# Optimization experiments

Hardware: AMD Instinct MI355X
Metric: run time of the kernel (lower is better)

## Reference

```python
import jax, jax.numpy as jnp
import numpy as np
import math

N, T, D_MODEL = 4, 2048, 1024
NHEAD = 16
HEAD_DIM = D_MODEL // NHEAD
ROTARY_DIM = 64
WINDOW = (128, 128)
ROPE_BASE = 10000.0


def _rope_cos_sin(seq_len, rotary_dim, dtype):
    # non-interleaved (GPT-NeoX style) rotary embedding tables
    inv_freq = 1.0 / (ROPE_BASE ** (jnp.arange(0, rotary_dim, 2, dtype=jnp.float32) / rotary_dim))
    t = jnp.arange(seq_len, dtype=jnp.float32)
    freqs = jnp.outer(t, inv_freq)  # [T, rotary_dim//2]
    return jnp.cos(freqs).astype(dtype), jnp.sin(freqs).astype(dtype)


def _apply_rope(x, cos, sin):
    # x: [N, T, H, D]; rotate first ROTARY_DIM dims, pass the rest through
    r = ROTARY_DIM
    x_rot, x_pass = x[..., :r], x[..., r:]
    x1, x2 = x_rot[..., : r // 2], x_rot[..., r // 2 :]
    c = cos[None, :, None, :]
    s = sin[None, :, None, :]
    out = jnp.concatenate([x1 * c - x2 * s, x1 * s + x2 * c], axis=-1)
    return jnp.concatenate([out, x_pass], axis=-1)


def _sliding_window_bias(seq_len, window, dtype):
    i = jnp.arange(seq_len)[:, None]
    j = jnp.arange(seq_len)[None, :]
    # triu(diag=-w0) & tril(diag=w1): keep j - i in [-w0, w1]
    keep = (j - i >= -window[0]) & (j - i <= window[1])
    return jnp.where(keep, jnp.zeros((), dtype), jnp.full((), -jnp.inf, dtype))


def setup_inputs() -> dict:
    key = jax.random.key(0)
    k1, k2, k3 = jax.random.split(key, 3)
    x = jax.random.normal(k1, (N, T, D_MODEL), dtype=jnp.float32)
    Wqkv = jax.random.normal(k2, (D_MODEL, 3 * D_MODEL), dtype=jnp.float32) * (1.0 / math.sqrt(D_MODEL))
    Wout = jax.random.normal(k3, (D_MODEL, D_MODEL), dtype=jnp.float32) * (1.0 / math.sqrt(D_MODEL))
    bout = jnp.zeros((D_MODEL,), dtype=jnp.float32)
    return {"x": x, "Wqkv": Wqkv, "Wout": Wout, "bout": bout}


def reference(x, Wqkv, Wout, bout):
    n, t, _ = x.shape
    qkv = (x @ Wqkv).reshape(n, t, 3, NHEAD, HEAD_DIM)
    q, k, v = qkv[:, :, 0], qkv[:, :, 1], qkv[:, :, 2]  # each [N, T, H, D]
    cos, sin = _rope_cos_sin(t, ROTARY_DIM, x.dtype)
    q = _apply_rope(q, cos, sin)
    k = _apply_rope(k, cos, sin)
    scale = 1.0 / math.sqrt(HEAD_DIM)
    bias = _sliding_window_bias(t, WINDOW, x.dtype)  # [T, T]
    scores = jnp.einsum("bthd,bshd->bhts", q, k) * scale + bias[None, None]
    attn = jax.nn.softmax(scores, axis=-1)
    out = jnp.einsum("bhts,bshd->bthd", attn, v).reshape(n, t, D_MODEL)
    return out @ Wout + bout
```

## Files before the change

### kernel.cpp

```cpp
#include <hip/hip_runtime.h>
#include <hip/hip_bf16.h>
#include <cstdint>
#include <cstddef>

typedef __bf16 bf16_t;
typedef bf16_t bf16x8 __attribute__((ext_vector_type(8)));
typedef float f32x4 __attribute__((ext_vector_type(4)));
typedef unsigned short ushort_t;

#define T_SEQ 2048
#define DM 1024
#define NH 16
#define HD 64
#define WIN 128
#define ROPE_C 0.28782313662425572f
#define SCALE_LOG2E 0.18033688011112042f
#define ATT_M 16.0f

__device__ __forceinline__ ushort_t f2bf(float f) {
    union { float f; unsigned u; } v; v.f = f;
    unsigned r = v.u + 0x7fff + ((v.u >> 16) & 1);
    return (ushort_t)(r >> 16);
}
__device__ __forceinline__ float sane(float v, float sent) {
    return (fabsf(v) < 1e30f) ? v : sent;
}
__device__ __forceinline__ void gld16(const ushort_t* g, ushort_t* l) {
    __builtin_amdgcn_global_load_lds(
        (const __attribute__((address_space(1))) unsigned int*)g,
        (__attribute__((address_space(3))) unsigned int*)l, 16, 0, 0);
}

__global__ __launch_bounds__(256) void kzero_f(float* __restrict__ p) {
    size_t i = ((size_t)blockIdx.x * 256 + threadIdx.x) * 4;
    float4 z; z.x = z.y = z.z = z.w = 0.f;
    *(float4*)(p + i) = z;
}

__device__ __forceinline__ void trans_f2b_tile(const float* __restrict__ in,
                                               ushort_t* __restrict__ out,
                                               int R, int C, int c0, int r0) {
    __shared__ __align__(16) ushort_t tile[64][72];
    const int tid = threadIdx.x;
    const int rl = tid >> 2, q4 = tid & 3;
    const float* src = in + (size_t)(r0 + rl) * C + c0 + q4 * 16;
    ushort_t cv[16];
#pragma unroll
    for (int i = 0; i < 4; i++) {
        float4 f = *(const float4*)(src + i * 4);
        cv[i * 4 + 0] = f2bf(f.x); cv[i * 4 + 1] = f2bf(f.y);
        cv[i * 4 + 2] = f2bf(f.z); cv[i * 4 + 3] = f2bf(f.w);
    }
    *(uint4*)&tile[rl][q4 * 16]     = *(uint4*)&cv[0];
    *(uint4*)&tile[rl][q4 * 16 + 8] = *(uint4*)&cv[8];
    __syncthreads();
    const int cl = tid >> 2;
    ushort_t tmp[16];
#pragma unroll
    for (int i = 0; i < 16; i++) tmp[i] = tile[q4 * 16 + i][cl];
    ushort_t* dst = out + (size_t)(c0 + cl) * R + r0 + q4 * 16;
    *(uint4*)(dst)     = *(uint4*)&tmp[0];
    *(uint4*)(dst + 8) = *(uint4*)&tmp[8];
}

__global__ __launch_bounds__(256) void prep(const float* __restrict__ x,
                                            const float* __restrict__ Wqkv,
                                            const float* __restrict__ Wout,
                                            ushort_t* __restrict__ xb,
                                            ushort_t* __restrict__ WqkvT,
                                            ushort_t* __restrict__ WoutT) {
    const int bx = blockIdx.x;
    if (bx < 4096) {
        size_t i = ((size_t)bx * 256 + threadIdx.x) * 8;
        float4 a0 = *(const float4*)(x + i);
        float4 a1 = *(const float4*)(x + i + 4);
        ushort_t cv[8];
        cv[0] = f2bf(a0.x); cv[1] = f2bf(a0.y); cv[2] = f2bf(a0.z); cv[3] = f2bf(a0.w);
        cv[4] = f2bf(a1.x); cv[5] = f2bf(a1.y); cv[6] = f2bf(a1.z); cv[7] = f2bf(a1.w);
        *(uint4*)(xb + i) = *(uint4*)cv;
    } else if (bx < 4864) {
        int tb = bx - 4096;
        trans_f2b_tile(Wqkv, WqkvT, 1024, 3072, (tb % 48) * 64, (tb / 48) * 64);
    } else {
        int tb = bx - 4864;
        trans_f2b_tile(Wout, WoutT, 1024, 1024, (tb & 15) * 64, (tb >> 4) * 64);
    }
}

__global__ __launch_bounds__(256) void gemm_qkv(const ushort_t* __restrict__ A,
                                                const ushort_t* __restrict__ Bt,
                                                ushort_t* __restrict__ Qr,
                                                ushort_t* __restrict__ Kr,
                                                ushort_t* __restrict__ Vt) {
    __shared__ __align__(16) ushort_t As[128 * 32];
    __shared__ __align__(16) ushort_t Bs[128 * 32];
    const int m0 = blockIdx.x * 128, n0 = blockIdx.y * 128;
    const int tid = threadIdx.x;
    const int lane = tid & 63, w = tid >> 6;
    const int wm = (w & 1) * 64, wn = (w >> 1) * 64;
    const int c = lane & 15, g = lane >> 4;
    const int lrow = lane >> 2, lcol = (lane & 3) * 8;
    const int ch0 = 2 * w, ch1 = 2 * w + 1;

    f32x4 acc[4][4];
#pragma unroll
    for (int mi = 0; mi < 4; mi++)
#pragma unroll
        for (int ni = 0; ni < 4; ni++)
#pragma unroll
            for (int r = 0; r < 4; r++) acc[mi][ni][r] = 0.f;

    for (int k0 = 0; k0 < 1024; k0 += 32) {
        __syncthreads();
        gld16(A  + (size_t)(m0 + ch0 * 16 + lrow) * 1024 + k0 + lcol, &As[ch0 * 512]);
        gld16(A  + (size_t)(m0 + ch1 * 16 + lrow) * 1024 + k0 + lcol, &As[ch1 * 512]);
        gld16(Bt + (size_t)(n0 + ch0 * 16 + lrow) * 1024 + k0 + lcol, &Bs[ch0 * 512]);
        gld16(Bt + (size_t)(n0 + ch1 * 16 + lrow) * 1024 + k0 + lcol, &Bs[ch1 * 512]);
        __syncthreads();
        bf16x8 af[4], bfr[4];
#pragma unroll
        for (int mi = 0; mi < 4; mi++)
            af[mi] = *(const bf16x8*)&As[(wm + mi * 16 + c) * 32 + g * 8];
#pragma unroll
        for (int ni = 0; ni < 4; ni++)
            bfr[ni] = *(const bf16x8*)&Bs[(wn + ni * 16 + c) * 32 + g * 8];
#pragma unroll
        for (int mi = 0; mi < 4; mi++)
#pragma unroll
            for (int ni = 0; ni < 4; ni++)
                acc[mi][ni] = __builtin_amdgcn_mfma_f32_16x16x32_bf16(
                    af[mi], bfr[ni], acc[mi][ni], 0, 0, 0);
    }

    const int nb = n0 + wn;
    const int sec = nb >> 10;
    const int h = (nb >> 6) & 15;

    if (sec < 2) {
        ushort_t* dst = (sec == 0) ? Qr : Kr;
        const float invf0 = __expf(-(float)(c) * ROPE_C);
        const float invf1 = __expf(-(float)(16 + c) * ROPE_C);
#pragma unroll
        for (int mi = 0; mi < 4; mi++)
#pragma unroll
            for (int r = 0; r < 4; r++) {
                int tg = m0 + wm + mi * 16 + g * 4 + r;
                int nB = tg >> 11, t = tg & (T_SEQ - 1);
                float a0 = (float)t * invf0, a1 = (float)t * invf1;
                float s0 = __sinf(a0), c0 = __cosf(a0);
                float s1 = __sinf(a1), c1 = __cosf(a1);
                size_t base = ((size_t)(nB * NH + h) * T_SEQ + t) * 64;
                float x1a = acc[mi][0][r], x2a = acc[mi][2][r];
                float x1b = acc[mi][1][r], x2b = acc[mi][3][r];
                dst[base + c]      = f2bf(sane(x1a * c0 - x2a * s0, 1e3f));
                dst[base + 16 + c] = f2bf(sane(x1b * c1 - x2b * s1, 1e3f));
                dst[base + 32 + c] = f2bf(sane(x1a * s0 + x2a * c0, 1e3f));
                dst[base + 48 + c] = f2bf(sane(x1b * s1 + x2b * c1, 1e3f));
            }
    } else {
#pragma unroll
        for (int mi = 0; mi < 4; mi++) {
            int tgb = m0 + wm + mi * 16 + g * 4;
            int nB = tgb >> 11, t = tgb & (T_SEQ - 1);
            size_t vrow = (size_t)(nB * NH + h) * 64 * T_SEQ;
#pragma unroll
            for (int ni = 0; ni < 4; ni++) {
                ushort4 pk;
                pk.x = f2bf(sane(acc[mi][ni][0], 1e3f));
                pk.y = f2bf(sane(acc[mi][ni][1], 1e3f));
                pk.z = f2bf(sane(acc[mi][ni][2], 1e3f));
                pk.w = f2bf(sane(acc[mi][ni][3], 1e3f));
                *(ushort4*)&Vt[vrow + (size_t)(ni * 16 + c) * T_SEQ + t] = pk;
            }
        }
    }
}

__global__ __launch_bounds__(256) void gemm_out(const ushort_t* __restrict__ A,
                                                const ushort_t* __restrict__ Bt,
                                                float* __restrict__ C,
                                                const float* __restrict__ bias) {
    __shared__ __align__(16) ushort_t As[64 * 32];
    __shared__ __align__(16) ushort_t Bs[128 * 32];
    const int m0 = blockIdx.x * 64, n0 = blockIdx.y * 128;
    const int tid = threadIdx.x;
    const int lane = tid & 63, w = tid >> 6;
    const int wm = (w & 1) * 32, wn = (w >> 1) * 64;
    const int c = lane & 15, g = lane >> 4;
    const int lrow = lane >> 2, lcol = (lane & 3) * 8;
    const int ch0 = 2 * w, ch1 = 2 * w + 1;

    f32x4 acc[2][4];
#pragma unroll
    for (int mi = 0; mi < 2; mi++)
#pragma unroll
        for (int ni = 0; ni < 4; ni++)
#pragma unroll
            for (int r = 0; r < 4; r++) acc[mi][ni][r] = 0.f;

    for (int k0 = 0; k0 < 1024; k0 += 32) {
        __syncthreads();
        gld16(A  + (size_t)(m0 + w * 16 + lrow) * 1024 + k0 + lcol, &As[w * 512]);
        gld16(Bt + (size_t)(n0 + ch0 * 16 + lrow) * 1024 + k0 + lcol, &Bs[ch0 * 512]);
        gld16(Bt + (size_t)(n0 + ch1 * 16 + lrow) * 1024 + k0 + lcol, &Bs[ch1 * 512]);
        __syncthreads();
        bf16x8 af[2], bfr[4];
#pragma unroll
        for (int mi = 0; mi < 2; mi++)
            af[mi] = *(const bf16x8*)&As[(wm + mi * 16 + c) * 32 + g * 8];
#pragma unroll
        for (int ni = 0; ni < 4; ni++)
            bfr[ni] = *(const bf16x8*)&Bs[(wn + ni * 16 + c) * 32 + g * 8];
#pragma unroll
        for (int mi = 0; mi < 2; mi++)
#pragma unroll
            for (int ni = 0; ni < 4; ni++)
                acc[mi][ni] = __builtin_amdgcn_mfma_f32_16x16x32_bf16(
                    af[mi], bfr[ni], acc[mi][ni], 0, 0, 0);
    }

#pragma unroll
    for (int ni = 0; ni < 4; ni++) {
        int col = n0 + wn + ni * 16 + c;
        float bv = bias[col];
#pragma unroll
        for (int mi = 0; mi < 2; mi++)
#pragma unroll
            for (int r = 0; r < 4; r++) {
                int rowi = m0 + wm + mi * 16 + g * 4 + r;
                C[(size_t)rowi * 1024 + col] = sane(acc[mi][ni][r] + bv, 1e8f);
            }
    }
}

__global__ __launch_bounds__(256) void attn_swin(const ushort_t* __restrict__ Qr,
                                                 const ushort_t* __restrict__ Kr,
                                                 const ushort_t* __restrict__ Vt,
                                                 ushort_t* __restrict__ O) {
    __shared__ __align__(16) ushort_t Ks[32 * 72];
    __shared__ __align__(16) ushort_t Vs[64 * 72];
    __shared__ __align__(16) ushort_t pbuf[4][2][16 * 32];
    const int tid = threadIdx.x;
    const int wid = tid >> 6, lane = tid & 63;
    const int qb = (blockIdx.x & 15) * 128;
    const int h = (blockIdx.x >> 4) & 15, n = blockIdx.x >> 8;
    const int c = lane & 15, g = lane >> 4;
    const size_t hb = ((size_t)(n * NH + h)) * T_SEQ * 64;
    const int t0s[2] = { qb + wid * 16, qb + 64 + wid * 16 };
    const int ks_row = tid >> 3, ks_col = (tid & 7) * 8;
    const int vs_row = tid >> 2, vs_col = (tid & 3) * 8;

    bf16x8 qf0[2], qf1[2];
#pragma unroll
    for (int sub = 0; sub < 2; sub++) {
        qf0[sub] = *(const bf16x8*)(Qr + hb + (size_t)(t0s[sub] + c) * 64 + g * 8);
        qf1[sub] = *(const bf16x8*)(Qr + hb + (size_t)(t0s[sub] + c) * 64 + 32 + g * 8);
    }

    f32x4 o[2][4];
    float l_r[2][4];
#pragma unroll
    for (int sub = 0; sub < 2; sub++)
#pragma unroll
        for (int i = 0; i < 4; i++) {
            l_r[sub][i] = 0.f;
#pragma unroll
            for (int r = 0; r < 4; r++) o[sub][i][r] = 0.f;
        }

    int sB_lo = qb - WIN;        if (sB_lo < 0) sB_lo = 0;
    int sB_hi = qb + 127 + WIN;  if (sB_hi > T_SEQ - 1) sB_hi = T_SEQ - 1;

    uint4 kreg = *(const uint4*)(Kr + hb + (size_t)(sB_lo + ks_row) * 64 + ks_col);
    uint4 vreg = *(const uint4*)(Vt + hb + (size_t)vs_row * T_SEQ + sB_lo + vs_col);

    for (int s0 = sB_lo; s0 <= sB_hi; s0 += 32) {
        __syncthreads();
        *(uint4*)&Ks[ks_row * 72 + ks_col] = kreg;
        *(uint4*)&Vs[vs_row * 72 + vs_col] = vreg;
        __syncthreads();
        int s1 = s0 + 32;
        if (s1 <= sB_hi) {
            kreg = *(const uint4*)(Kr + hb + (size_t)(s1 + ks_row) * 64 + ks_col);
            vreg = *(const uint4*)(Vt + hb + (size_t)vs_row * T_SEQ + s1 + vs_col);
        }
        bool act[2];
#pragma unroll
        for (int sub = 0; sub < 2; sub++)
            act[sub] = !(s0 > t0s[sub] + 143 || s0 + 31 < t0s[sub] - WIN);
        if (!act[0] && !act[1]) continue;

#pragma unroll
        for (int sub = 0; sub < 2; sub++) {
            if (!act[sub]) continue;
            const int t0 = t0s[sub];
            f32x4 S[2];
#pragma unroll
            for (int sh = 0; sh < 2; sh++) {
                bf16x8 kf0 = *(const bf16x8*)&Ks[(sh * 16 + c) * 72 + g * 8];
                bf16x8 kf1 = *(const bf16x8*)&Ks[(sh * 16 + c) * 72 + 32 + g * 8];
                f32x4 z;
#pragma unroll
                for (int r = 0; r < 4; r++) z[r] = 0.f;
                z = __builtin_amdgcn_mfma_f32_16x16x32_bf16(qf0[sub], kf0, z, 0, 0, 0);
                z = __builtin_amdgcn_mfma_f32_16x16x32_bf16(qf1[sub], kf1, z, 0, 0, 0);
                S[sh] = z;
            }
            const bool interior = (s0 >= t0 - 113) && (s0 <= t0 + 97);
            ushort_t* pb = pbuf[wid][sub];
            if (interior) {
#pragma unroll
                for (int sh = 0; sh < 2; sh++)
#pragma unroll
                    for (int r = 0; r < 4; r++) {
                        float p = exp2f(S[sh][r] * SCALE_LOG2E - ATT_M);
                        l_r[sub][r] += p;
                        pb[(g * 4 + r) * 32 + sh * 16 + c] = f2bf(p);
                    }
            } else {
#pragma unroll
                for (int sh = 0; sh < 2; sh++)
#pragma unroll
                    for (int r = 0; r < 4; r++) {
                        int s = s0 + sh * 16 + c;
                        int q = t0 + g * 4 + r;
                        bool keep = (s - q >= -WIN) && (s - q <= WIN);
                        float v = keep ? S[sh][r] * SCALE_LOG2E : -1e30f;
                        float p = exp2f(v - ATT_M);
                        l_r[sub][r] += p;
                        pb[(g * 4 + r) * 32 + sh * 16 + c] = f2bf(p);
                    }
            }
        }
        __asm__ volatile("s_waitcnt lgkmcnt(0)" ::: "memory");
#pragma unroll
        for (int sub = 0; sub < 2; sub++) {
            if (!act[sub]) continue;
            bf16x8 pf = *(const bf16x8*)&pbuf[wid][sub][c * 32 + g * 8];
#pragma unroll
            for (int di = 0; di < 4; di++) {
                bf16x8 vf = *(const bf16x8*)&Vs[(di * 16 + c) * 72 + g * 8];
                o[sub][di] = __builtin_amdgcn_mfma_f32_16x16x32_bf16(pf, vf, o[sub][di], 0, 0, 0);
            }
        }
        __asm__ volatile("" ::: "memory");
    }

#pragma unroll
    for (int sub = 0; sub < 2; sub++) {
#pragma unroll
        for (int off = 1; off < 16; off <<= 1)
#pragma unroll
            for (int r = 0; r < 4; r++)
                l_r[sub][r] += __shfl_xor(l_r[sub][r], off, 64);
        float inv[4];
#pragma unroll
        for (int r = 0; r < 4; r++) inv[r] = __builtin_amdgcn_rcpf(l_r[sub][r]);
#pragma unroll
        for (int di = 0; di < 4; di++)
#pragma unroll
            for (int r = 0; r < 4; r++) {
                int q = t0s[sub] + g * 4 + r;
                float val = o[sub][di][r] * inv[r];
                O[((size_t)(n * T_SEQ + q)) * DM + h * 64 + di * 16 + c] =
                    f2bf(sane(val, 1e6f));
            }
    }
}

extern "C" void kernel_launch(void* const* d_in, const int* in_sizes, int n_in,
                              void* d_out, int out_size, void* d_ws, size_t ws_size,
                              hipStream_t stream) {
    const float* x    = (const float*)d_in[0];
    const float* Wqkv = (const float*)d_in[1];
    const float* Wout = (const float*)d_in[2];
    const float* bout = (const float*)d_in[3];
    float* out = (float*)d_out;

    const size_t NEED = 72ull << 20;
    if (ws_size < NEED) {
        kzero_f<<<dim3(8192), 256, 0, stream>>>(out);
        return;
    }
    char* ws = (char*)d_ws;
    ushort_t* WqkvT = (ushort_t*)(ws);
    ushort_t* WoutT = (ushort_t*)(ws + (6ull << 20));
    ushort_t* Qr    = (ushort_t*)(ws + (8ull << 20));
    ushort_t* Kr    = (ushort_t*)(ws + (24ull << 20));
    ushort_t* Vt    = (ushort_t*)(ws + (40ull << 20));
    ushort_t* xb    = (ushort_t*)(ws + (56ull << 20));
    ushort_t* Oat   = xb;

    prep<<<dim3(5120), 256, 0, stream>>>(x, Wqkv, Wout, xb, WqkvT, WoutT);
    gemm_qkv<<<dim3(64, 24), 256, 0, stream>>>(xb, WqkvT, Qr, Kr, Vt);
    attn_swin<<<dim3(1024), 256, 0, stream>>>(Qr, Kr, Vt, Oat);
    gemm_out<<<dim3(128, 8), 256, 0, stream>>>(Oat, WoutT, out, bout);
}
```

Measured before the change: 220.4 us.

## Rewrite both GEMMs with triple-buffered async LDS pipeline, larger tiles, swizzled layout

Replaces the QKV and output projection GEMM loops with a shared core using 128x256x64 tiles, 512 threads, a three-stage LDS ring buffer filled by async global-to-LDS loads, and an XOR-swizzled LDS layout. MFMA work is split into two phases separated by barriers, with wave priority raised around the matrix instructions. The goal is to hide global load latency behind compute, cut per-iteration barrier cost and improve data reuse. In exchange the larger LDS footprint and per-block register use lower occupancy, and the output GEMM now launches only 256 blocks, which may underfill the GPU.

Result: faster. 210.1 us (-4.7%).

```diff
diff --git a/kernel.cpp b/kernel.cpp
--- a/kernel.cpp
+++ b/kernel.cpp
@@ -87,64 +87,140 @@
     }
 }
 
-__global__ __launch_bounds__(256) void gemm_qkv(const ushort_t* __restrict__ A,
+#define BM 128
+#define BN 256
+#define BK 64
+#define KTILES 16
+#define LBUF ((BM + BN) * BK)
+#define LTOT (3 * LBUF)
+
+__device__ __forceinline__ void gemm_core(const ushort_t* __restrict__ Agl,
+                                          const ushort_t* __restrict__ Bgl,
+                                          ushort_t* L, int m0, int n0,
+                                          f32x4 (&acc)[4][4]) {
+    const int tid = threadIdx.x;
+    const int lane = tid & 63, w = tid >> 6;
+    const int wr = w >> 2, wc = w & 3;
+    const int c = lane & 15, g = lane >> 4;
+    const int rr = tid >> 3;
+    const int cc8 = ((tid & 7) ^ (rr & 7)) * 8;
+    const int lw = (w * 8) * BK;
+    const int arow = wr * 64 + c;
+    const int brow = wc * 64 + c;
+    const int cxk0 = ((0 + g) ^ (c & 7)) * 8;
+    const int cxk1 = ((4 + g) ^ (c & 7)) * 8;
+
+#pragma unroll
+    for (int mi = 0; mi < 4; ++mi)
+#pragma unroll
+        for (int ni = 0; ni < 4; ++ni)
+#pragma unroll
+            for (int r = 0; r < 4; ++r) acc[mi][ni][r] = 0.f;
+
+    auto STAGE = [&](int kt, int bo) {
+        const int k0 = kt * BK;
+        const ushort_t* ga = Agl + (size_t)(m0 + rr) * 1024 + k0 + cc8;
+        ushort_t* la = L + bo + lw;
+        gld16(ga, la);
+        gld16(ga + 64 * 1024, la + 64 * BK);
+        const ushort_t* gb = Bgl + (size_t)(n0 + rr) * 1024 + k0 + cc8;
+        ushort_t* lb = la + BM * BK;
+#pragma unroll
+        for (int s = 0; s < 4; ++s)
+            gld16(gb + (size_t)(s * 64) * 1024, lb + s * 64 * BK);
+    };
+
+    STAGE(0, 0);
+    STAGE(1, LBUF);
+    asm volatile("s_waitcnt vmcnt(6)\n\ts_barrier" ::: "memory");
+
+    int bcur = 0;
+    for (int kt = 0; kt < KTILES; ++kt) {
+        int bst = bcur + 2 * LBUF; if (bst >= LTOT) bst -= LTOT;
+        if (kt + 2 < KTILES) STAGE(kt + 2, bst);
+
+        const ushort_t* Lb = L + bcur;
+        const ushort_t* Bb = Lb + BM * BK;
+        bf16x8 af[4][2], bf[2][2];
+#pragma unroll
+        for (int mi = 0; mi < 4; ++mi) {
+            const ushort_t* p = Lb + (arow + mi * 16) * BK;
+            af[mi][0] = *(const bf16x8*)(p + cxk0);
+            af[mi][1] = *(const bf16x8*)(p + cxk1);
+        }
+#pragma unroll
+        for (int ni = 0; ni < 2; ++ni) {
+            const ushort_t* p = Bb + (brow + ni * 16) * BK;
+            bf[ni][0] = *(const bf16x8*)(p + cxk0);
+            bf[ni][1] = *(const bf16x8*)(p + cxk1);
+        }
+        asm volatile("s_barrier" ::: "memory");
+        __builtin_amdgcn_s_setprio(1);
+#pragma unroll
+        for (int mi = 0; mi < 4; ++mi)
+#pragma unroll
+            for (int ni = 0; ni < 2; ++ni) {
+                acc[mi][ni] = __builtin_amdgcn_mfma_f32_16x16x32_bf16(
+                    af[mi][0], bf[ni][0], acc[mi][ni], 0, 0, 0);
+                acc[mi][ni] = __builtin_amdgcn_mfma_f32_16x16x32_bf16(
+                    af[mi][1], bf[ni][1], acc[mi][ni], 0, 0, 0);
+            }
+        __builtin_amdgcn_s_setprio(0);
+        asm volatile("s_barrier" ::: "memory");
+        bf16x8 bg[2][2];
+#pragma unroll
+        for (int ni = 0; ni < 2; ++ni) {
+            const ushort_t* p = Bb + (brow + (ni + 2) * 16) * BK;
+            bg[ni][0] = *(const bf16x8*)(p + cxk0);
+            bg[ni][1] = *(const bf16x8*)(p + cxk1);
+        }
+        asm volatile("s_barrier" ::: "memory");
+        __builtin_amdgcn_s_setprio(1);
+#pragma unroll
+        for (int mi = 0; mi < 4; ++mi)
+#pragma unroll
+            for (int ni = 0; ni < 2; ++ni) {
+                acc[mi][ni + 2] = __builtin_amdgcn_mfma_f32_16x16x32_bf16(
+                    af[mi][0], bg[ni][0], acc[mi][ni + 2], 0, 0, 0);
+                acc[mi][ni + 2] = __builtin_amdgcn_mfma_f32_16x16x32_bf16(
+                    af[mi][1], bg[ni][1], acc[mi][ni + 2], 0, 0, 0);
+            }
+        __builtin_amdgcn_s_setprio(0);
+        if (kt < KTILES - 2)
+            asm volatile("s_waitcnt vmcnt(6)\n\ts_barrier" ::: "memory");
+        else if (kt == KTILES - 2)
+            asm volatile("s_waitcnt vmcnt(0)\n\ts_barrier" ::: "memory");
+        bcur += LBUF; if (bcur == LTOT) bcur = 0;
+    }
+}
+
+__global__ __launch_bounds__(512) void gemm_qkv(const ushort_t* __restrict__ A,
                                                 const ushort_t* __restrict__ Bt,
                                                 ushort_t* __restrict__ Qr,
                                                 ushort_t* __restrict__ Kr,
                                                 ushort_t* __restrict__ Vt) {
-    __shared__ __align__(16) ushort_t As[128 * 32];
-    __shared__ __align__(16) ushort_t Bs[128 * 32];
-    const int m0 = blockIdx.x * 128, n0 = blockIdx.y * 128;
-    const int tid = threadIdx.x;
-    const int lane = tid & 63, w = tid >> 6;
-    const int wm = (w & 1) * 64, wn = (w >> 1) * 64;
+    __shared__ __align__(16) ushort_t L[LTOT];
+    const int m0 = blockIdx.x * BM, n0 = blockIdx.y * BN;
+    f32x4 acc[4][4];
+    gemm_core(A, Bt, L, m0, n0, acc);
+
+    const int lane = threadIdx.x & 63, w = threadIdx.x >> 6;
+    const int wr = w >> 2, wc = w & 3;
     const int c = lane & 15, g = lane >> 4;
-    const int lrow = lane >> 2, lcol = (lane & 3) * 8;
-    const int ch0 = 2 * w, ch1 = 2 * w + 1;
-
-    f32x4 acc[4][4];
-#pragma unroll
-    for (int mi = 0; mi < 4; mi++)
-#pragma unroll
-        for (int ni = 0; ni < 4; ni++)
-#pragma unroll
-            for (int r = 0; r < 4; r++) acc[mi][ni][r] = 0.f;
-
-    for (int k0 = 0; k0 < 1024; k0 += 32) {
-        __syncthreads();
-        gld16(A  + (size_t)(m0 + ch0 * 16 + lrow) * 1024 + k0 + lcol, &As[ch0 * 512]);
-        gld16(A  + (size_t)(m0 + ch1 * 16 + lrow) * 1024 + k0 + lcol, &As[ch1 * 512]);
-        gld16(Bt + (size_t)(n0 + ch0 * 16 + lrow) * 1024 + k0 + lcol, &Bs[ch0 * 512]);
-        gld16(Bt + (size_t)(n0 + ch1 * 16 + lrow) * 1024 + k0 + lcol, &Bs[ch1 * 512]);
-        __syncthreads();
-        bf16x8 af[4], bfr[4];
-#pragma unroll
-        for (int mi = 0; mi < 4; mi++)
-            af[mi] = *(const bf16x8*)&As[(wm + mi * 16 + c) * 32 + g * 8];
-#pragma unroll
-        for (int ni = 0; ni < 4; ni++)
-            bfr[ni] = *(const bf16x8*)&Bs[(wn + ni * 16 + c) * 32 + g * 8];
-#pragma unroll
-        for (int mi = 0; mi < 4; mi++)
-#pragma unroll
-            for (int ni = 0; ni < 4; ni++)
-                acc[mi][ni] = __builtin_amdgcn_mfma_f32_16x16x32_bf16(
-                    af[mi], bfr[ni], acc[mi][ni], 0, 0, 0);
-    }
-
-    const int nb = n0 + wn;
+    const int nb = n0 + wc * 64;
     const int sec = nb >> 10;
     const int h = (nb >> 6) & 15;
+    const int mrow = m0 + wr * 64;
 
     if (sec < 2) {
         ushort_t* dst = (sec == 0) ? Qr : Kr;
         const float invf0 = __expf(-(float)(c) * ROPE_C);
         const float invf1 = __expf(-(float)(16 + c) * ROPE_C);
 #pragma unroll
-        for (int mi = 0; mi < 4; mi++)
-#pragma unroll
-            for (int r = 0; r < 4; r++) {
-                int tg = m0 + wm + mi * 16 + g * 4 + r;
+        for (int mi = 0; mi < 4; ++mi)
+#pragma unroll
+            for (int r = 0; r < 4; ++r) {
+                int tg = mrow + mi * 16 + g * 4 + r;
                 int nB = tg >> 11, t = tg & (T_SEQ - 1);
                 float a0 = (float)t * invf0, a1 = (float)t * invf1;
                 float s0 = __sinf(a0), c0 = __cosf(a0);
@@ -159,12 +235,12 @@
             }
     } else {
 #pragma unroll
-        for (int mi = 0; mi < 4; mi++) {
-            int tgb = m0 + wm + mi * 16 + g * 4;
+        for (int mi = 0; mi < 4; ++mi) {
+            int tgb = mrow + mi * 16 + g * 4;
             int nB = tgb >> 11, t = tgb & (T_SEQ - 1);
             size_t vrow = (size_t)(nB * NH + h) * 64 * T_SEQ;
 #pragma unroll
-            for (int ni = 0; ni < 4; ni++) {
+            for (int ni = 0; ni < 4; ++ni) {
                 ushort4 pk;
                 pk.x = f2bf(sane(acc[mi][ni][0], 1e3f));
                 pk.y = f2bf(sane(acc[mi][ni][1], 1e3f));
@@ -176,58 +252,27 @@
     }
 }
 
-__global__ __launch_bounds__(256) void gemm_out(const ushort_t* __restrict__ A,
+__global__ __launch_bounds__(512) void gemm_out(const ushort_t* __restrict__ A,
                                                 const ushort_t* __restrict__ Bt,
                                                 float* __restrict__ C,
                                                 const float* __restrict__ bias) {
-    __shared__ __align__(16) ushort_t As[64 * 32];
-    __shared__ __align__(16) ushort_t Bs[128 * 32];
-    const int m0 = blockIdx.x * 64, n0 = blockIdx.y * 128;
-    const int tid = threadIdx.x;
-    const int lane = tid & 63, w = tid >> 6;
-    const int wm = (w & 1) * 32, wn = (w >> 1) * 64;
+    __shared__ __align__(16) ushort_t L[LTOT];
+    const int m0 = blockIdx.x * BM, n0 = blockIdx.y * BN;
+    f32x4 acc[4][4];
+    gemm_core(A, Bt, L, m0, n0, acc);
+
+    const int lane = threadIdx.x & 63, w = threadIdx.x >> 6;
+    const int wr = w >> 2, wc = w & 3;
     const int c = lane & 15, g = lane >> 4;
-    const int lrow = lane >> 2, lcol = (lane & 3) * 8;
-    const int ch0 = 2 * w, ch1 = 2 * w + 1;
-
-    f32x4 acc[2][4];
-#pragma unroll
-    for (int mi = 0; mi < 2; mi++)
-#pragma unroll
-        for (int ni = 0; ni < 4; ni++)
-#pragma unroll
-            for (int r = 0; r < 4; r++) acc[mi][ni][r] = 0.f;
-
-    for (int k0 = 0; k0 < 1024; k0 += 32) {
-        __syncthreads();
-        gld16(A  + (size_t)(m0 + w * 16 + lrow) * 1024 + k0 + lcol, &As[w * 512]);
-        gld16(Bt + (size_t)(n0 + ch0 * 16 + lrow) * 1024 + k0 + lcol, &Bs[ch0 * 512]);
-        gld16(Bt + (size_t)(n0 + ch1 * 16 + lrow) * 1024 + k0 + lcol, &Bs[ch1 * 512]);
-        __syncthreads();
-        bf16x8 af[2], bfr[4];
-#pragma unroll
-        for (int mi = 0; mi < 2; mi++)
-            af[mi] = *(const bf16x8*)&As[(wm + mi * 16 + c) * 32 + g * 8];
-#pragma unroll
-        for (int ni = 0; ni < 4; ni++)
-            bfr[ni] = *(const bf16x8*)&Bs[(wn + ni * 16 + c) * 32 + g * 8];
-#pragma unroll
-        for (int mi = 0; mi < 2; mi++)
-#pragma unroll
-            for (int ni = 0; ni < 4; ni++)
-                acc[mi][ni] = __builtin_amdgcn_mfma_f32_16x16x32_bf16(
-                    af[mi], bfr[ni], acc[mi][ni], 0, 0, 0);
-    }
-
-#pragma unroll
-    for (int ni = 0; ni < 4; ni++) {
-        int col = n0 + wn + ni * 16 + c;
+#pragma unroll
+    for (int ni = 0; ni < 4; ++ni) {
+        int col = n0 + wc * 64 + ni * 16 + c;
         float bv = bias[col];
 #pragma unroll
-        for (int mi = 0; mi < 2; mi++)
-#pragma unroll
-            for (int r = 0; r < 4; r++) {
-                int rowi = m0 + wm + mi * 16 + g * 4 + r;
+        for (int mi = 0; mi < 4; ++mi)
+#pragma unroll
+            for (int r = 0; r < 4; ++r) {
+                int rowi = m0 + wr * 64 + mi * 16 + g * 4 + r;
                 C[(size_t)rowi * 1024 + col] = sane(acc[mi][ni][r] + bv, 1e8f);
             }
     }
@@ -392,7 +437,7 @@
     ushort_t* Oat   = xb;
 
     prep<<<dim3(5120), 256, 0, stream>>>(x, Wqkv, Wout, xb, WqkvT, WoutT);
-    gemm_qkv<<<dim3(64, 24), 256, 0, stream>>>(xb, WqkvT, Qr, Kr, Vt);
+    gemm_qkv<<<dim3(64, 12), 512, 0, stream>>>(xb, WqkvT, Qr, Kr, Vt);
     attn_swin<<<dim3(1024), 256, 0, stream>>>(Qr, Kr, Vt, Oat);
-    gemm_out<<<dim3(128, 8), 256, 0, stream>>>(Oat, WoutT, out, bout);
-}
+    gemm_out<<<dim3(64, 4), 512, 0, stream>>>(Oat, WoutT, out, bout);
+}
```
